# Performance work log

Hardware: AMD Instinct MI355X
Metric: run time of the kernel (lower is better)

The kernel has to match this reference:

```python
import jax, jax.numpy as jnp
import numpy as np

K_TOP = 4  # C_output
EPS = 1e-5


def setup_inputs() -> dict:
    N, C, H = 3072, 16, 128
    key = jax.random.key(0)
    ks = jax.random.split(key, 6)
    s = 1.0 / np.sqrt(H)
    return {
        "input_embedding": jax.random.normal(ks[0], (N, C, H), jnp.float32),
        "W1": jax.random.normal(ks[1], (H, H), jnp.float32) * s,
        "b1": jnp.zeros((H,), jnp.float32),
        "ln_g": jnp.ones((H,), jnp.float32),
        "ln_b": jnp.zeros((H,), jnp.float32),
        "W2": jax.random.normal(ks[2], (1, H), jnp.float32) * s,
        "b2": jnp.zeros((1,), jnp.float32),
        "sage_Wl": jax.random.normal(ks[3], (C, H, H), jnp.float32) * s,
        "sage_bl": jnp.zeros((C, H), jnp.float32),
        "sage_Wr": jax.random.normal(ks[4], (C, H, H), jnp.float32) * s,
    }


def _forward(input_embedding, W1, b1, ln_g, ln_b, W2, b2, sage_Wl, sage_bl, sage_Wr):
    n, c, h = input_embedding.shape
    # ---- feature importance learner (single shared MLP, dropout in eval) ----
    z = jax.nn.relu(jnp.einsum('nch,oh->nco', input_embedding, W1) + b1)
    mu = z.mean(-1, keepdims=True)
    var = z.var(-1, keepdims=True)  # biased, matches torch LayerNorm
    z = (z - mu) / jnp.sqrt(var + EPS) * ln_g + ln_b
    fi = jax.nn.softmax((jnp.einsum('nch,oh->nco', z, W2) + b2)[..., 0], axis=1)  # [N,C]

    feat = input_embedding * fi[:, :, None]  # importance-weighted embeddings [N,C,H]

    # ---- top-K column routing per row ----
    _, topk_idx = jax.lax.top_k(fi, K_TOP)                                    # [N,K]
    mask = jnp.zeros((n, c), bool).at[jnp.arange(n)[:, None], topk_idx].set(True)
    imp = jax.nn.softmax(jnp.where(mask, fi, -1e9), axis=1)                   # [N,C]

    col_ids = jnp.arange(c)

    # ---- per-column dynamic graph + SAGEConv (scan over C columns) ----
    def col_step(_, xs):
        ci, feat_c, cmask, Wl, bl, Wr = xs  # feat_c [N,H], cmask [N] bool
        cm = cmask.astype(feat_c.dtype)
        # subset rows whose topK contains column ci; zero out column ci
        Mc = jnp.where(col_ids[None, :] == ci, 0.0, imp) * cm[:, None]        # [N,C]
        A = (Mc @ Mc.T > 0).astype(feat_c.dtype)                              # [N,N] edges
        deg = A.sum(axis=1)
        agg = (A @ feat_c) / jnp.maximum(deg, 1.0)[:, None]                   # mean aggr
        hc = agg @ Wl.T + bl + feat_c @ Wr.T                                  # SAGEConv
        hc = jax.nn.relu(hc)
        # torch.layer_norm(x, x.shape): normalize over the whole subset tensor
        m = cm[:, None]
        n_el = jnp.maximum(cm.sum() * h, 1.0)
        mu_ = (hc * m).sum() / n_el
        var_ = (((hc - mu_) ** 2) * m).sum() / n_el
        hc = (hc - mu_) / jnp.sqrt(var_ + EPS)
        return None, hc

    _, H_all = jax.lax.scan(
        col_step, None,
        (col_ids, feat.transpose(1, 0, 2), mask.T, sage_Wl, sage_bl, sage_Wr))  # [C,N,H]

    # ---- regroup: per row, its K routed columns in ascending column order ----
    cols_sorted = jnp.sort(topk_idx, axis=1)                                  # [N,K]
    out = H_all[cols_sorted, jnp.arange(n)[:, None], :]                       # [N,K,H]
    return out


def reference(input_embedding, W1, b1, ln_g, ln_b, W2, b2, sage_Wl, sage_bl, sage_Wr):
    return _forward(input_embedding, W1, b1, ln_g, ln_b, W2, b2,
                    sage_Wl, sage_bl, sage_Wr)
```

## Files before the change

### kernel.cpp

```cpp
#include <hip/hip_runtime.h>

#define NN 3072
#define CCC 16
#define HH 128
#define KTOP 4
#define NCLS 455
#define EPSF 1e-5f

#define OFF_F       0
#define SZ_F        (16*NCLS*HH)
#define OFF_CNT     (OFF_F + SZ_F)
#define SZ_CNT      (16*NCLS)
#define OFF_SUMS    (OFF_CNT + SZ_CNT)
#define SZ_SUMS     32
#define OFF_NCNT    (OFF_SUMS + SZ_SUMS)
#define SZ_NCNT     256
#define SMALL_ZERO  (SZ_CNT + SZ_SUMS + SZ_NCNT)
#define OFF_COLS    (OFF_NCNT + SZ_NCNT)
#define SZ_E        (NN*KTOP)
#define OFF_RANKS   (OFF_COLS + SZ_E)
#define OFF_FISEL   (OFF_RANKS + SZ_E)
#define OFF_NLIST   (OFF_FISEL + SZ_E)
#define SZ_NLIST    (16*NN)
#define OFF_AGG     (OFF_NLIST + SZ_NLIST)
#define OFF_HC      (OFF_AGG + SZ_F)
#define SZ_HC       (NN*KTOP*HH)
#define OFF_HALF    (OFF_HC + SZ_HC)
#define HOFF_W1H    0
#define HOFF_W1L    16384
#define HOFF_WLH    32768
#define HOFF_WRH    (32768 + 262144)

#define MT 64
#define GCP 8
#define GCB (HH/GCP)

typedef _Float16 h8 __attribute__((ext_vector_type(8)));
typedef float    f4 __attribute__((ext_vector_type(4)));

__device__ __forceinline__ int C2i(int x){ return x*(x-1)/2; }
__device__ __forceinline__ int C3i(int x){ return x*(x-1)*(x-2)/6; }

__global__ __launch_bounds__(256) void k_cvt(const float* __restrict__ W1,
    _Float16* __restrict__ hbase, float* __restrict__ ws){
  int i = blockIdx.x*256 + threadIdx.x;
  if (i < 16384){
    float x = W1[i];
    _Float16 h = (_Float16)x;
    hbase[HOFF_W1H + i] = h;
    hbase[HOFF_W1L + i] = (_Float16)(x - (float)h);
  }
  if (i < SMALL_ZERO) ws[OFF_CNT + i] = 0.f;
}

__global__ __launch_bounds__(256) void k_fused(const float* __restrict__ X,
    const _Float16* __restrict__ W1h, const _Float16* __restrict__ W1l,
    const float* __restrict__ b1, const float* __restrict__ ln_g,
    const float* __restrict__ ln_b, const float* __restrict__ W2,
    const float* __restrict__ b2,
    const float* __restrict__ Wl, const float* __restrict__ Wr,
    _Float16* __restrict__ hbase, float* __restrict__ F,
    int* __restrict__ cols, int* __restrict__ ranks, float* __restrict__ fiSel){
  __shared__ float llog[64];
  int t = threadIdx.x;
  int w = t >> 6;
  int lane = t & 63;
  int l15 = lane & 15, quad = lane >> 4;
  int base = blockIdx.x * MT;
  int mA = base + 16*w + l15;

  {
    f4 z4 = (f4){0.f,0.f,0.f,0.f};
    for (int i = blockIdx.x*256 + t; i < SZ_F/4; i += 768*256)
      *(f4*)(F + (size_t)i*4) = z4;
    for (int i = blockIdx.x*256 + t; i < 2*262144; i += 768*256){
      if (i < 262144) hbase[HOFF_WLH + i] = (_Float16)Wl[i];
      else            hbase[HOFF_WRH + (i-262144)] = (_Float16)Wr[i-262144];
    }
  }

  const float* xrow = X + (size_t)mA*HH;
  h8 ah[4], al[4];
  #pragma unroll
  for (int c=0;c<4;++c){
    float4 u = *(const float4*)(xrow + c*32 + quad*8);
    float4 v = *(const float4*)(xrow + c*32 + quad*8 + 4);
    float xv[8] = {u.x,u.y,u.z,u.w,v.x,v.y,v.z,v.w};
    #pragma unroll
    for (int j=0;j<8;++j){
      _Float16 hi = (_Float16)xv[j];
      ah[c][j] = hi;
      al[c][j] = (_Float16)(xv[j] - (float)hi);
    }
  }

  f4 acc[8];
  #pragma unroll
  for (int nt=0;nt<8;++nt) acc[nt] = (f4){0.f,0.f,0.f,0.f};

  #pragma unroll
  for (int c=0;c<4;++c){
    #pragma unroll
    for (int nt=0;nt<8;++nt){
      int o = nt*16 + l15;
      h8 bh  = *(const h8*)(W1h + (size_t)o*HH + c*32 + quad*8);
      h8 bl_ = *(const h8*)(W1l + (size_t)o*HH + c*32 + quad*8);
      acc[nt] = __builtin_amdgcn_mfma_f32_16x16x32_f16(ah[c], bh,  acc[nt], 0,0,0);
      acc[nt] = __builtin_amdgcn_mfma_f32_16x16x32_f16(al[c], bh,  acc[nt], 0,0,0);
      acc[nt] = __builtin_amdgcn_mfma_f32_16x16x32_f16(ah[c], bl_, acc[nt], 0,0,0);
      acc[nt] = __builtin_amdgcn_mfma_f32_16x16x32_f16(al[c], bl_, acc[nt], 0,0,0);
    }
  }

  float bv[8], gv[8], lv[8], wv[8];
  #pragma unroll
  for (int nt=0;nt<8;++nt){
    int o = nt*16 + l15;
    bv[nt]=b1[o]; gv[nt]=ln_g[o]; lv[nt]=ln_b[o]; wv[nt]=W2[o];
  }
  float b2v = b2[0];
  #pragma unroll
  for (int r=0;r<4;++r){
    float z[8];
    float s1=0.f, s2=0.f;
    #pragma unroll
    for (int nt=0;nt<8;++nt){
      float zz = acc[nt][r] + bv[nt];
      zz = zz>0.f ? zz : 0.f;
      z[nt] = zz; s1 += zz; s2 += zz*zz;
    }
    #pragma unroll
    for (int m=1;m<16;m<<=1){ s1 += __shfl_xor(s1,m); s2 += __shfl_xor(s2,m); }
    float mu = s1/(float)HH;
    float var = s2/(float)HH - mu*mu;
    float rs = 1.0f/sqrtf(var+EPSF);
    float s3 = 0.f;
    #pragma unroll
    for (int nt=0;nt<8;++nt){
      float zn = (z[nt]-mu)*rs*gv[nt] + lv[nt];
      s3 += zn*wv[nt];
    }
    #pragma unroll
    for (int m=1;m<16;m<<=1) s3 += __shfl_xor(s3,m);
    if (l15 == 0) llog[16*w + quad*4 + r] = s3 + b2v;
  }
  __syncthreads();

  if (t < 4){
    int n = blockIdx.x*4 + t;
    float l[CCC];
    #pragma unroll
    for (int c=0;c<CCC;++c) l[c] = llog[t*16+c];
    unsigned mask = 0;
    #pragma unroll
    for (int k=0;k<KTOP;++k){
      float best = -3e38f; int bi = 0;
      #pragma unroll
      for (int c=0;c<CCC;++c){
        bool taken = (mask>>c)&1u;
        if (!taken && l[c] > best){ best = l[c]; bi = c; }
      }
      mask |= 1u<<bi;
    }
    float m = -3e38f;
    #pragma unroll
    for (int c=0;c<CCC;++c) m = l[c]>m ? l[c] : m;
    float s = 0.f;
    #pragma unroll
    for (int c=0;c<CCC;++c) s += expf(l[c]-m);
    float inv = 1.0f/s;
    unsigned m2 = mask;
    for (int j=0;j<KTOP;++j){
      int ci = __ffs(m2)-1; m2 &= m2-1u;
      unsigned rest = mask & ~(1u<<ci);
      int v[3]; unsigned r2 = rest;
      #pragma unroll
      for (int q=0;q<3;++q){ int col = __ffs(r2)-1; r2 &= r2-1u; v[q] = col - (col>ci ? 1:0); }
      int rank = C3i(v[2]) + C2i(v[1]) + v[0];
      int e4 = n*KTOP + j;
      cols[e4] = ci; ranks[e4] = rank; fiSel[e4] = expf(l[ci]-m)*inv;
    }
  }
}

__global__ __launch_bounds__(256) void k_nlist(const int* __restrict__ cols,
    int* __restrict__ nodeCnt, int* __restrict__ nodeList){
  __shared__ int lcnt[CCC];
  __shared__ int lbase[CCC];
  int t = threadIdx.x;
  if (t < CCC) lcnt[t] = 0;
  __syncthreads();
  int n = blockIdx.x*256 + t;
  int mycis[KTOP], mypos[KTOP];
  #pragma unroll
  for (int j=0;j<KTOP;++j){
    int ci = cols[n*KTOP+j];
    mycis[j] = ci;
    mypos[j] = atomicAdd(&lcnt[ci], 1);
  }
  __syncthreads();
  if (t < CCC) lbase[t] = atomicAdd(&nodeCnt[t*16], lcnt[t]);
  __syncthreads();
  #pragma unroll
  for (int j=0;j<KTOP;++j){
    int ci = mycis[j];
    nodeList[ci*NN + lbase[ci] + mypos[j]] = n*KTOP + j;
  }
}

__global__ __launch_bounds__(256) void k_accF(const float* __restrict__ X,
    const int* __restrict__ cols, const int* __restrict__ ranks,
    const float* __restrict__ fiSel, float* __restrict__ F, float* __restrict__ cnt){
  int e = blockIdx.x*2 + (threadIdx.x>>7);
  int h = threadIdx.x & 127;
  int ci = cols[e], rank = ranks[e];
  float fi = fiSel[e];
  int n = e >> 2;
  float v = X[(n*CCC+ci)*HH + h] * fi;
  atomicAdd(&F[(ci*NCLS+rank)*HH + h], v);
  if (h==0) atomicAdd(&cnt[ci*NCLS+rank], 1.0f);
}

__global__ __launch_bounds__(256) void k_graph(const float* __restrict__ F,
    const float* __restrict__ cnt, float* __restrict__ agg){
  int cb = blockIdx.x, ci = blockIdx.y, t = threadIdx.x;
  __shared__ float cntl[NCLS];
  __shared__ float PcS[105], UcS[15];
  __shared__ int   abcs[NCLS];
  __shared__ int   prs[NCLS];
  __shared__ float Fl[NCLS*GCP];
  __shared__ float P[105*GCP];
  __shared__ float U[15*GCP];
  const float* Fc = F + (size_t)ci*NCLS*HH + cb*GCP;

  for (int i=t; i<NCLS*2; i+=256){
    int r = i>>1, hf = i&1;
    float4 v = *(const float4*)(Fc + (size_t)r*HH + hf*4);
    *(float4*)(&Fl[r*GCP + hf*4]) = v;
  }
  for (int r=t; r<NCLS; r+=256){
    cntl[r] = cnt[ci*NCLS+r];
    int c=2; while (c<14 && C3i(c+1)<=r) c++;
    int rem = r - C3i(c);
    int b=1; while (b<c-1 && C2i(b+1)<=rem) b++;
    int a = rem - C2i(b);
    abcs[r] = a | (b<<5) | (c<<10);
    prs[r] = (C2i(b)+a) | ((C2i(c)+a)<<10) | ((C2i(c)+b)<<20);
  }
  __syncthreads();
  if (t<105){
    int pb=1; while (pb<14 && C2i(pb+1)<=t) pb++;
    int pa = t - C2i(pb);
    float s=0.f;
    #pragma unroll
    for (int z=0;z<15;++z){
      if (z==pa||z==pb) continue;
      int lo,mid,hi;
      if (z<pa){lo=z;mid=pa;hi=pb;} else if (z<pb){lo=pa;mid=z;hi=pb;} else {lo=pa;mid=pb;hi=z;}
      s += cntl[C3i(hi)+C2i(mid)+lo];
    }
    PcS[t]=s;
  }
  __syncthreads();
  if (t<15){
    float s=0.f;
    #pragma unroll
    for (int y=0;y<15;++y){
      if (y==t) continue;
      int lo = t<y?t:y, hi = t<y?y:t;
      s += PcS[C2i(hi)+lo];
    }
    UcS[t]=0.5f*s;
  }
  __syncthreads();
  for (int idx=t; idx<105*GCP; idx+=256){
    int p = idx/GCP, col = idx&(GCP-1);
    int pb=1; while (pb<14 && C2i(pb+1)<=p) pb++;
    int pa = p - C2i(pb);
    float s=0.f;
    #pragma unroll
    for (int z=0;z<15;++z){
      if (z==pa||z==pb) continue;
      int lo,mid,hi;
      if (z<pa){lo=z;mid=pa;hi=pb;} else if (z<pb){lo=pa;mid=z;hi=pb;} else {lo=pa;mid=pb;hi=z;}
      s += Fl[(C3i(hi)+C2i(mid)+lo)*GCP + col];
    }
    P[idx]=s;
  }
  __syncthreads();
  for (int idx=t; idx<15*GCP; idx+=256){
    int x = idx/GCP, col = idx&(GCP-1);
    float s=0.f;
    #pragma unroll
    for (int y=0;y<15;++y){
      if (y==x) continue;
      int lo = x<y?x:y, hi = x<y?y:x;
      s += P[(C2i(hi)+lo)*GCP + col];
    }
    U[idx]=0.5f*s;
  }
  __syncthreads();
  for (int idx=t; idx<NCLS*GCP; idx+=256){
    int r = idx/GCP, col = idx&(GCP-1);
    int v1=abcs[r]; int a=v1&31,b=(v1>>5)&31,c=(v1>>10)&31;
    int v2=prs[r];  int pab=v2&1023,pac=(v2>>10)&1023,pbc=(v2>>20)&1023;
    float deg = UcS[a]+UcS[b]+UcS[c]-PcS[pab]-PcS[pac]-PcS[pbc]+cntl[r];
    float invd = 1.0f/fmaxf(deg,1.0f);
    float v = U[a*GCP+col]+U[b*GCP+col]+U[c*GCP+col]
            - P[pab*GCP+col]-P[pac*GCP+col]-P[pbc*GCP+col]
            + Fl[r*GCP+col];
    agg[(size_t)ci*NCLS*HH + (size_t)r*HH + cb*GCP + col] = v*invd;
  }
}

__global__ __launch_bounds__(256) void k_aggwl(float* __restrict__ agg,
    const _Float16* __restrict__ Wlh, const float* __restrict__ bl){
  int t = threadIdx.x;
  int w = t >> 6;
  int lane = t & 63;
  int l15 = lane & 15, quad = lane >> 4;
  int ci = blockIdx.y;
  int base = blockIdx.x * MT;
  int rowA = base + 16*w + l15; if (rowA > NCLS-1) rowA = NCLS-1;

  const float* arow = agg + ((size_t)ci*NCLS + rowA)*HH;
  h8 af[4];
  #pragma unroll
  for (int c=0;c<4;++c){
    float4 u = *(const float4*)(arow + c*32 + quad*8);
    float4 v = *(const float4*)(arow + c*32 + quad*8 + 4);
    float xv[8] = {u.x,u.y,u.z,u.w,v.x,v.y,v.z,v.w};
    #pragma unroll
    for (int j=0;j<8;++j) af[c][j] = (_Float16)xv[j];
  }

  f4 acc[8];
  #pragma unroll
  for (int nt=0;nt<8;++nt) acc[nt] = (f4){0.f,0.f,0.f,0.f};

  const _Float16* Wc = Wlh + (size_t)ci*HH*HH;
  #pragma unroll
  for (int c=0;c<4;++c){
    #pragma unroll
    for (int nt=0;nt<8;++nt){
      int o = nt*16 + l15;
      h8 bh = *(const h8*)(Wc + (size_t)o*HH + c*32 + quad*8);
      acc[nt] = __builtin_amdgcn_mfma_f32_16x16x32_f16(af[c], bh, acc[nt], 0,0,0);
    }
  }
  #pragma unroll
  for (int r=0;r<4;++r){
    int row2 = base + 16*w + quad*4 + r;
    if (row2 < NCLS){
      float* drow = agg + ((size_t)ci*NCLS + row2)*HH;
      #pragma unroll
      for (int nt=0;nt<8;++nt){
        int o = nt*16 + l15;
        drow[o] = acc[nt][r] + bl[ci*HH + o];
      }
    }
  }
}

__global__ __launch_bounds__(256) void k_hc2(const float* __restrict__ X,
    const _Float16* __restrict__ Wrh,
    const int* __restrict__ ranks, const float* __restrict__ fiSel,
    const int* __restrict__ nodeCnt, const int* __restrict__ nodeList,
    const float* __restrict__ aggwl, float* __restrict__ hcBuf, float* __restrict__ sums){
  int ci = blockIdx.y;
  int cntc = nodeCnt[ci*16];
  int base = blockIdx.x * MT;
  if (base >= cntc) return;
  __shared__ float rb[8];
  int t = threadIdx.x;
  int w = t >> 6;
  int lane = t & 63;
  int l15 = lane & 15, quad = lane >> 4;

  int pA = base + 16*w + l15;
  float fi = 0.f; int nA = 0;
  if (pA < cntc){
    int e = nodeList[ci*NN + pA];
    fi = fiSel[e]; nA = e >> 2;
  }
  const float* xrow = X + ((size_t)nA*CCC + ci)*HH;
  h8 af[4];
  #pragma unroll
  for (int c=0;c<4;++c){
    float4 u = *(const float4*)(xrow + c*32 + quad*8);
    float4 v = *(const float4*)(xrow + c*32 + quad*8 + 4);
    float xv[8] = {u.x,u.y,u.z,u.w,v.x,v.y,v.z,v.w};
    #pragma unroll
    for (int j=0;j<8;++j) af[c][j] = (_Float16)(xv[j]*fi);
  }

  f4 acc[8];
  #pragma unroll
  for (int nt=0;nt<8;++nt) acc[nt] = (f4){0.f,0.f,0.f,0.f};

  const _Float16* Wc = Wrh + (size_t)ci*HH*HH;
  #pragma unroll
  for (int c=0;c<4;++c){
    #pragma unroll
    for (int nt=0;nt<8;++nt){
      int o = nt*16 + l15;
      h8 bh = *(const h8*)(Wc + (size_t)o*HH + c*32 + quad*8);
      acc[nt] = __builtin_amdgcn_mfma_f32_16x16x32_f16(af[c], bh, acc[nt], 0,0,0);
    }
  }

  float s1 = 0.f, s2 = 0.f;
  #pragma unroll
  for (int r=0;r<4;++r){
    int pD = base + 16*w + quad*4 + r;
    int e2 = -1, rk2 = 0;
    if (pD < cntc){ e2 = nodeList[ci*NN + pD]; rk2 = ranks[e2]; }
    if (e2 >= 0){
      const float* G = aggwl + ((size_t)ci*NCLS + rk2)*HH;
      float* drow = hcBuf + (size_t)e2*HH;
      #pragma unroll
      for (int nt=0;nt<8;++nt){
        int o = nt*16 + l15;
        float vv = acc[nt][r] + G[o];
        vv = vv>0.f ? vv : 0.f;
        drow[o] = vv;
        s1 += vv; s2 += vv*vv;
      }
    }
  }
  #pragma unroll
  for (int m=1;m<64;m<<=1){ s1 += __shfl_xor(s1,m); s2 += __shfl_xor(s2,m); }
  if (lane == 0){ rb[w] = s1; rb[4+w] = s2; }
  __syncthreads();
  if (t==0){
    atomicAdd(&sums[ci],    rb[0]+rb[1]+rb[2]+rb[3]);
    atomicAdd(&sums[16+ci], rb[4]+rb[5]+rb[6]+rb[7]);
  }
}

__global__ __launch_bounds__(256) void k_out(const float* __restrict__ hcBuf,
    const int* __restrict__ cols, const int* __restrict__ nodeCnt,
    const float* __restrict__ sums, float* __restrict__ out){
  int idx = blockIdx.x*256 + threadIdx.x;
  int e = idx >> 7;
  int ci = cols[e];
  float cntf = (float)nodeCnt[ci*16];
  float nel = fmaxf(cntf * (float)HH, 1.0f);
  float mu = sums[ci]/nel;
  float var = sums[16+ci]/nel - mu*mu;
  out[idx] = (hcBuf[idx]-mu)/sqrtf(var+EPSF);
}

extern "C" void kernel_launch(void* const* d_in, const int* in_sizes, int n_in,
                              void* d_out, int out_size, void* d_ws, size_t ws_size,
                              hipStream_t stream){
  const float* X    = (const float*)d_in[0];
  const float* W1   = (const float*)d_in[1];
  const float* b1   = (const float*)d_in[2];
  const float* ln_g = (const float*)d_in[3];
  const float* ln_b = (const float*)d_in[4];
  const float* W2   = (const float*)d_in[5];
  const float* b2   = (const float*)d_in[6];
  const float* Wl   = (const float*)d_in[7];
  const float* bl   = (const float*)d_in[8];
  const float* Wr   = (const float*)d_in[9];
  float* ws = (float*)d_ws;
  float* F      = ws + OFF_F;
  float* cnt    = ws + OFF_CNT;
  float* sums   = ws + OFF_SUMS;
  int*   nodeCnt= (int*)(ws + OFF_NCNT);
  int*   cols   = (int*)(ws + OFF_COLS);
  int*   ranks  = (int*)(ws + OFF_RANKS);
  float* fiSel  = ws + OFF_FISEL;
  int*   nodeList=(int*)(ws + OFF_NLIST);
  float* agg    = ws + OFF_AGG;
  float* hcBuf  = ws + OFF_HC;
  _Float16* hbase = (_Float16*)(ws + OFF_HALF);
  float* out    = (float*)d_out;

  k_cvt    <<<dim3(64), dim3(256), 0, stream>>>(W1, hbase, ws);
  k_fused  <<<dim3(NN*CCC/MT), dim3(256), 0, stream>>>(X, hbase+HOFF_W1H, hbase+HOFF_W1L,
                                                       b1, ln_g, ln_b, W2, b2, Wl, Wr,
                                                       hbase, F, cols, ranks, fiSel);
  k_nlist  <<<dim3(NN/256), dim3(256), 0, stream>>>(cols, nodeCnt, nodeList);
  k_accF   <<<dim3(NN*KTOP/2), dim3(256), 0, stream>>>(X, cols, ranks, fiSel, F, cnt);
  k_graph  <<<dim3(GCB,16), dim3(256), 0, stream>>>(F, cnt, agg);
  k_aggwl  <<<dim3((NCLS+MT-1)/MT,16), dim3(256), 0, stream>>>(agg, hbase+HOFF_WLH, bl);
  k_hc2    <<<dim3((NN/MT),16), dim3(256), 0, stream>>>(X, hbase+HOFF_WRH, ranks, fiSel,
                                                        nodeCnt, nodeList, agg, hcBuf, sums);
  k_out    <<<dim3(NN*KTOP*HH/256), dim3(256), 0, stream>>>(hcBuf, cols, nodeCnt, sums, out);
}
```

Measured before the change: 175.5 us.

## Fold W1 split conversion and small-buffer zeroing into k_fused, merge nlist into accF

Removes the separate k_cvt launch. Each k_fused block now converts W1 into padded hi/lo fp16 tiles in shared memory and reads its MFMA B operands from LDS instead of global memory, and block 0 zeroes the count, sum and node-count buffers. The node-list build is merged into k_accF as 12 extra blocks, which removes another launch. The cost is that each of the 768 blocks redundantly converts the full 128x128 W1 and uses about 67KB of LDS, which may lower occupancy.

```diff
diff --git a/kernel.cpp b/kernel.cpp
--- a/kernel.cpp
+++ b/kernel.cpp
@@ -26,14 +26,13 @@
 #define OFF_HC      (OFF_AGG + SZ_F)
 #define SZ_HC       (NN*KTOP*HH)
 #define OFF_HALF    (OFF_HC + SZ_HC)
-#define HOFF_W1H    0
-#define HOFF_W1L    16384
-#define HOFF_WLH    32768
-#define HOFF_WRH    (32768 + 262144)
+#define HOFF_WLH    0
+#define HOFF_WRH    262144
 
 #define MT 64
 #define GCP 8
 #define GCB (HH/GCP)
+#define W1P 132
 
 typedef _Float16 h8 __attribute__((ext_vector_type(8)));
 typedef float    f4 __attribute__((ext_vector_type(4)));
@@ -41,26 +40,16 @@
 __device__ __forceinline__ int C2i(int x){ return x*(x-1)/2; }
 __device__ __forceinline__ int C3i(int x){ return x*(x-1)*(x-2)/6; }
 
-__global__ __launch_bounds__(256) void k_cvt(const float* __restrict__ W1,
-    _Float16* __restrict__ hbase, float* __restrict__ ws){
-  int i = blockIdx.x*256 + threadIdx.x;
-  if (i < 16384){
-    float x = W1[i];
-    _Float16 h = (_Float16)x;
-    hbase[HOFF_W1H + i] = h;
-    hbase[HOFF_W1L + i] = (_Float16)(x - (float)h);
-  }
-  if (i < SMALL_ZERO) ws[OFF_CNT + i] = 0.f;
-}
-
 __global__ __launch_bounds__(256) void k_fused(const float* __restrict__ X,
-    const _Float16* __restrict__ W1h, const _Float16* __restrict__ W1l,
+    const float* __restrict__ W1,
     const float* __restrict__ b1, const float* __restrict__ ln_g,
     const float* __restrict__ ln_b, const float* __restrict__ W2,
     const float* __restrict__ b2,
     const float* __restrict__ Wl, const float* __restrict__ Wr,
-    _Float16* __restrict__ hbase, float* __restrict__ F,
+    _Float16* __restrict__ hbase, float* __restrict__ F, float* __restrict__ ws,
     int* __restrict__ cols, int* __restrict__ ranks, float* __restrict__ fiSel){
+  __shared__ _Float16 w1h_s[HH*W1P];
+  __shared__ _Float16 w1l_s[HH*W1P];
   __shared__ float llog[64];
   int t = threadIdx.x;
   int w = t >> 6;
@@ -69,6 +58,14 @@
   int base = blockIdx.x * MT;
   int mA = base + 16*w + l15;
 
+  for (int j = t; j < HH*HH; j += 256){
+    int r = j >> 7, c0 = j & 127;
+    float x = W1[j];
+    _Float16 h = (_Float16)x;
+    w1h_s[r*W1P + c0] = h;
+    w1l_s[r*W1P + c0] = (_Float16)(x - (float)h);
+  }
+
   {
     f4 z4 = (f4){0.f,0.f,0.f,0.f};
     for (int i = blockIdx.x*256 + t; i < SZ_F/4; i += 768*256)
@@ -77,6 +74,8 @@
       if (i < 262144) hbase[HOFF_WLH + i] = (_Float16)Wl[i];
       else            hbase[HOFF_WRH + (i-262144)] = (_Float16)Wr[i-262144];
     }
+    if (blockIdx.x == 0)
+      for (int i = t; i < SMALL_ZERO; i += 256) ws[OFF_CNT + i] = 0.f;
   }
 
   const float* xrow = X + (size_t)mA*HH;
@@ -93,6 +92,7 @@
       al[c][j] = (_Float16)(xv[j] - (float)hi);
     }
   }
+  __syncthreads();
 
   f4 acc[8];
   #pragma unroll
@@ -103,8 +103,8 @@
     #pragma unroll
     for (int nt=0;nt<8;++nt){
       int o = nt*16 + l15;
-      h8 bh  = *(const h8*)(W1h + (size_t)o*HH + c*32 + quad*8);
-      h8 bl_ = *(const h8*)(W1l + (size_t)o*HH + c*32 + quad*8);
+      h8 bh  = *(const h8*)(w1h_s + o*W1P + c*32 + quad*8);
+      h8 bl_ = *(const h8*)(w1l_s + o*W1P + c*32 + quad*8);
       acc[nt] = __builtin_amdgcn_mfma_f32_16x16x32_f16(ah[c], bh,  acc[nt], 0,0,0);
       acc[nt] = __builtin_amdgcn_mfma_f32_16x16x32_f16(al[c], bh,  acc[nt], 0,0,0);
       acc[nt] = __builtin_amdgcn_mfma_f32_16x16x32_f16(ah[c], bl_, acc[nt], 0,0,0);
@@ -183,42 +183,43 @@
   }
 }
 
-__global__ __launch_bounds__(256) void k_nlist(const int* __restrict__ cols,
+__global__ __launch_bounds__(256) void k_accF(const float* __restrict__ X,
+    const int* __restrict__ cols, const int* __restrict__ ranks,
+    const float* __restrict__ fiSel, float* __restrict__ F, float* __restrict__ cnt,
     int* __restrict__ nodeCnt, int* __restrict__ nodeList){
   __shared__ int lcnt[CCC];
   __shared__ int lbase[CCC];
   int t = threadIdx.x;
-  if (t < CCC) lcnt[t] = 0;
-  __syncthreads();
-  int n = blockIdx.x*256 + t;
-  int mycis[KTOP], mypos[KTOP];
-  #pragma unroll
-  for (int j=0;j<KTOP;++j){
-    int ci = cols[n*KTOP+j];
-    mycis[j] = ci;
-    mypos[j] = atomicAdd(&lcnt[ci], 1);
-  }
-  __syncthreads();
-  if (t < CCC) lbase[t] = atomicAdd(&nodeCnt[t*16], lcnt[t]);
-  __syncthreads();
-  #pragma unroll
-  for (int j=0;j<KTOP;++j){
-    int ci = mycis[j];
-    nodeList[ci*NN + lbase[ci] + mypos[j]] = n*KTOP + j;
-  }
-}
-
-__global__ __launch_bounds__(256) void k_accF(const float* __restrict__ X,
-    const int* __restrict__ cols, const int* __restrict__ ranks,
-    const float* __restrict__ fiSel, float* __restrict__ F, float* __restrict__ cnt){
-  int e = blockIdx.x*2 + (threadIdx.x>>7);
-  int h = threadIdx.x & 127;
-  int ci = cols[e], rank = ranks[e];
-  float fi = fiSel[e];
-  int n = e >> 2;
-  float v = X[(n*CCC+ci)*HH + h] * fi;
-  atomicAdd(&F[(ci*NCLS+rank)*HH + h], v);
-  if (h==0) atomicAdd(&cnt[ci*NCLS+rank], 1.0f);
+  if (blockIdx.x < NN*KTOP/2){
+    int e = blockIdx.x*2 + (t>>7);
+    int h = t & 127;
+    int ci = cols[e], rank = ranks[e];
+    float fi = fiSel[e];
+    int n = e >> 2;
+    float v = X[(n*CCC+ci)*HH + h] * fi;
+    atomicAdd(&F[(ci*NCLS+rank)*HH + h], v);
+    if (h==0) atomicAdd(&cnt[ci*NCLS+rank], 1.0f);
+  } else {
+    int nb = blockIdx.x - NN*KTOP/2;
+    if (t < CCC) lcnt[t] = 0;
+    __syncthreads();
+    int n = nb*256 + t;
+    int mycis[KTOP], mypos[KTOP];
+    #pragma unroll
+    for (int j=0;j<KTOP;++j){
+      int ci = cols[n*KTOP+j];
+      mycis[j] = ci;
+      mypos[j] = atomicAdd(&lcnt[ci], 1);
+    }
+    __syncthreads();
+    if (t < CCC) lbase[t] = atomicAdd(&nodeCnt[t*16], lcnt[t]);
+    __syncthreads();
+    #pragma unroll
+    for (int j=0;j<KTOP;++j){
+      int ci = mycis[j];
+      nodeList[ci*NN + lbase[ci] + mypos[j]] = n*KTOP + j;
+    }
+  }
 }
 
 __global__ __launch_bounds__(256) void k_graph(const float* __restrict__ F,
@@ -478,12 +479,11 @@
   _Float16* hbase = (_Float16*)(ws + OFF_HALF);
   float* out    = (float*)d_out;
 
-  k_cvt    <<<dim3(64), dim3(256), 0, stream>>>(W1, hbase, ws);
-  k_fused  <<<dim3(NN*CCC/MT), dim3(256), 0, stream>>>(X, hbase+HOFF_W1H, hbase+HOFF_W1L,
-                                                       b1, ln_g, ln_b, W2, b2, Wl, Wr,
-                                                       hbase, F, cols, ranks, fiSel);
-  k_nlist  <<<dim3(NN/256), dim3(256), 0, stream>>>(cols, nodeCnt, nodeList);
-  k_accF   <<<dim3(NN*KTOP/2), dim3(256), 0, stream>>>(X, cols, ranks, fiSel, F, cnt);
+  k_fused  <<<dim3(NN*CCC/MT), dim3(256), 0, stream>>>(X, W1, b1, ln_g, ln_b, W2, b2,
+                                                       Wl, Wr, hbase, F, ws,
+                                                       cols, ranks, fiSel);
+  k_accF   <<<dim3(NN*KTOP/2 + 12), dim3(256), 0, stream>>>(X, cols, ranks, fiSel, F, cnt,
+                                                            nodeCnt, nodeList);
   k_graph  <<<dim3(GCB,16), dim3(256), 0, stream>>>(F, cnt, agg);
   k_aggwl  <<<dim3((NCLS+MT-1)/MT,16), dim3(256), 0, stream>>>(agg, hbase+HOFF_WLH, bl);
   k_hc2    <<<dim3((NN/MT),16), dim3(256), 0, stream>>>(X, hbase+HOFF_WRH, ranks, fiSel,
```

Measured after the change: 165.5 us. 1.06x faster.
